# Kernel optimization log

Hardware: AMD Instinct MI355X
Metric: run time of the kernel (lower is better)

Reference implementation:

```python
import jax, jax.numpy as jnp
import numpy as np
from jax import lax

DEPTH = 3  # signature truncation depth
B, L, I, H, O = 256, 512, 32, 16, 10
SIG_DIM = H + H**2 + H**3  # 4368 = signatory.signature_channels(16, 3)


def setup_inputs() -> dict:
    key = jax.random.key(0)
    ks = jax.random.split(key, 7)
    s = 1.0 / np.sqrt(H).astype(np.float32)
    sf = 1.0 / np.sqrt(SIG_DIM).astype(np.float32)
    return {
        "X": jax.random.normal(ks[0], (B, L, I), jnp.float32),
        "W_ih": jax.random.uniform(ks[1], (4 * H, I), jnp.float32, -s, s),
        "W_hh": jax.random.uniform(ks[2], (4 * H, H), jnp.float32, -s, s),
        "b_ih": jax.random.uniform(ks[3], (4 * H,), jnp.float32, -s, s),
        "b_hh": jax.random.uniform(ks[4], (4 * H,), jnp.float32, -s, s),
        "fc_w": jax.random.uniform(ks[5], (O, SIG_DIM), jnp.float32, -sf, sf),
        "fc_b": jax.random.uniform(ks[6], (O,), jnp.float32, -sf, sf),
    }


def _lstm(X, W_ih, W_hh, b_ih, b_hh):
    # torch nn.LSTM, single layer, batch_first, gate order (i, f, g, o)
    b, l, _ = X.shape
    h0 = jnp.zeros((b, H), X.dtype)
    c0 = jnp.zeros((b, H), X.dtype)
    # precompute input projection for all timesteps: [L, B, 4H]
    xw = jnp.swapaxes(jnp.einsum('bli,gi->blg', X, W_ih) + b_ih + b_hh, 0, 1)

    def step(carry, xw_t):
        h, c = carry
        gates = xw_t + h @ W_hh.T
        i, f, g, o = jnp.split(gates, 4, axis=-1)
        c = jax.nn.sigmoid(f) * c + jax.nn.sigmoid(i) * jnp.tanh(g)
        h = jax.nn.sigmoid(o) * jnp.tanh(c)
        return (h, c), h

    _, hs = lax.scan(step, (h0, c0), xw)  # hs: [L, B, H]
    return jnp.swapaxes(hs, 0, 1)  # [B, L, H]


def _outer(a, b):
    # batched flattened tensor product: [B, m] x [B, n] -> [B, m*n]
    return (a[:, :, None] * b[:, None, :]).reshape(a.shape[0], -1)


def _signature(h, depth):
    # signatory.signature: Chen's identity scan over path increments,
    # returns concatenated levels 1..depth: [B, C + C^2 + ... + C^depth]
    b, l, c = h.shape
    dx = jnp.swapaxes(h[:, 1:] - h[:, :-1], 0, 1)  # [L-1, B, C]
    S0 = tuple(jnp.zeros((b, c ** (k + 1)), h.dtype) for k in range(depth))

    def step(S, d):
        # exp(d) levels: e_k = d^{tensor k} / k!
        e = [d]
        for k in range(2, depth + 1):
            e.append(_outer(e[-1], d) / k)
        # S <- S (x) exp(d), truncated:  newS_k = S_k + sum_{j=1..k-1} S_{k-j} (x) e_j + e_k
        newS = []
        for k in range(1, depth + 1):
            acc = S[k - 1] + e[k - 1]
            for j in range(1, k):
                acc = acc + _outer(S[k - j - 1], e[j - 1])
            newS.append(acc)
        return tuple(newS), None

    S, _ = lax.scan(step, S0, dx)
    return jnp.concatenate(S, axis=-1)  # [B, SIG_DIM]


def reference(X, W_ih, W_hh, b_ih, b_hh, fc_w, fc_b):
    hseq = _lstm(X, W_ih, W_hh, b_ih, b_hh)           # [B, L, H]
    sig = _signature(hseq, DEPTH)                      # [B, SIG_DIM]
    out = sig @ fc_w.T + fc_b                          # [B, O]
    return out.reshape(-1, O)
```

## Files before the change

### kernel.cpp

```cpp
#include <hip/hip_runtime.h>

#define NB 256
#define NL 512
#define NI 32
#define NH 16
#define NG 64
#define SIGD 4368
#define XS 516

__device__ __forceinline__ float RL(float v, int lane) {
  return __builtin_bit_cast(float, __builtin_amdgcn_readlane(__builtin_bit_cast(int, v), lane));
}
template<int CTRL>
__device__ __forceinline__ float QB(float v) {
  return __builtin_bit_cast(float, __builtin_amdgcn_update_dpp(
      0, __builtin_bit_cast(int, v), CTRL, 0xF, 0xF, true));
}
__device__ __forceinline__ int cutf(int k) {
  switch (k) {
    case 1: return 24;  case 2: return 102; case 3: return 180; case 4: return 258;
    case 5: return 335; case 6: return 412; case 7: return 488; case 8: return 511;
    default: return 0;
  }
}

__global__ __launch_bounds__(512, 1) void k_main(const float* __restrict__ X,
    const float* __restrict__ Wih, const float* __restrict__ bih,
    const float* __restrict__ bhh, const float* __restrict__ Whh,
    const float* __restrict__ fcw, const float* __restrict__ fcb,
    float* __restrict__ out) {
  __shared__ __align__(16) float xwT[NG * XS];
  __shared__ __align__(16) float bnd[144];
  __shared__ int prog;
  int tid = threadIdx.x;
  int wv = tid >> 6;
  int ln = tid & 63;
  int b = blockIdx.x;

  if (tid == 0) prog = -1;

  {
    const float Kg = (ln >= 32 && ln < 48) ? 2.885390082f : -1.442695041f;
    float w2[NI];
#pragma unroll
    for (int i = 0; i < 8; ++i) {
      float4 v = *(const float4*)(Wih + ln * NI + 4 * i);
      w2[4*i+0] = v.x; w2[4*i+1] = v.y; w2[4*i+2] = v.z; w2[4*i+3] = v.w;
    }
    float bias = bih[ln] + bhh[ln];
    const float* xb = X + (size_t)b * NL * NI;
#pragma unroll 4
    for (int t = 64 * wv; t < 64 * (wv + 1); ++t) {
      const float4* xr = (const float4*)(xb + t * NI);
      float x0 = bias, x1 = 0.f, x2 = 0.f, x3 = 0.f;
#pragma unroll
      for (int i = 0; i < 8; ++i) {
        float4 xv = xr[i];
        x0 += xv.x * w2[4*i+0]; x1 += xv.y * w2[4*i+1];
        x2 += xv.z * w2[4*i+2]; x3 += xv.w * w2[4*i+3];
      }
      xwT[ln * XS + t] = Kg * ((x0 + x1) + (x2 + x3));
    }
  }
  __syncthreads();

  if (wv == 0) {
    __asm__ __volatile__("s_setprio 3");
    const int q = ln & 3;
    const int j = ln >> 2;
    const int gmem = q * 16 + j;
    const bool isg = (q == 2);
    const float Kg = isg ? 2.885390082f : -1.442695041f;
    const float Av = isg ? -2.0f : 1.0f;
    const float Bv = isg ? 1.0f : 0.0f;
    const float CT = 2.885390082f;
    float w[NH];
#pragma unroll
    for (int qq = 0; qq < 4; ++qq) {
      float4 v = *(const float4*)(Whh + gmem * NH + 4 * qq);
      w[4*qq+0] = Kg*v.x; w[4*qq+1] = Kg*v.y; w[4*qq+2] = Kg*v.z; w[4*qq+3] = Kg*v.w;
    }
    const float* xt = xwT + gmem * XS;
    float4 xq[4];
#pragma unroll
    for (int i = 0; i < 4; ++i) xq[i] = *(const float4*)(xt + 4 * i);
    float cs = 0.0f, hval = 0.0f;
    for (int tb = 0; tb < NL; tb += 16) {
#pragma unroll
      for (int k = 0; k < 16; ++k) {
        int t = tb + k;
        float hs[16];
#pragma unroll
        for (int u = 0; u < 16; ++u) hs[u] = RL(hval, 4 * u);
        float xval = ((const float*)xq)[k];
        if ((k & 3) == 3 && t + 16 < NL)
          xq[k >> 2] = *(const float4*)(xt + (t + 13));
        float a0 = xval, a1 = 0.f, a2 = 0.f, a3 = 0.f;
#pragma unroll
        for (int u = 0; u < 4; ++u) {
          a0 += hs[4*u+0] * w[4*u+0];
          a1 += hs[4*u+1] * w[4*u+1];
          a2 += hs[4*u+2] * w[4*u+2];
          a3 += hs[4*u+3] * w[4*u+3];
        }
        float acc = (a0 + a1) + (a2 + a3);
        float e = __builtin_amdgcn_exp2f(acc);
        float r = __builtin_amdgcn_rcpf(1.0f + e);
        float val = __builtin_fmaf(Av, r, Bv);
        float iv = QB<0x00>(val);
        float fv = QB<0x55>(val);
        float gv = QB<0xAA>(val);
        float ov = QB<0xFF>(val);
        cs = __builtin_fmaf(fv, cs, (CT * iv) * gv);
        float e2 = __builtin_amdgcn_exp2f(cs);
        float tc = __builtin_fmaf(-2.0f, __builtin_amdgcn_rcpf(1.0f + e2), 1.0f);
        hval = ov * tc;
        if (q == 0) xwT[j * XS + t] = hval;
      }
      __asm__ __volatile__("" ::: "memory");
      if (ln == 0) *(volatile int*)&prog = tb + 15;
    }
    __asm__ __volatile__("s_setprio 0");
  }

  const int bi = ln & 15;
  const int hi = ln >> 4;
  const int ch = wv;
  int ts = cutf(ch);
  int te = cutf(ch + 1);
  while (*(volatile int*)&prog < te) __builtin_amdgcn_s_sleep(8);
  __asm__ __volatile__("" ::: "memory");

  float s3[4][16];
  float s2[4] = {0.f, 0.f, 0.f, 0.f};
#pragma unroll
  for (int m = 0; m < 4; ++m)
#pragma unroll
    for (int cc = 0; cc < 16; ++cc) s3[m][cc] = 0.f;
  float hc[16];
#pragma unroll
  for (int cc = 0; cc < 16; ++cc) hc[cc] = xwT[cc * XS + ts];
  float hcb = xwT[bi * XS + ts];
  float hca[4], h0a[4];
#pragma unroll
  for (int m = 0; m < 4; ++m) { hca[m] = xwT[(4 * m + hi) * XS + ts]; h0a[m] = hca[m]; }
  for (int t = ts; t < te; ++t) {
    int tn = t + 1;
    float hn[16];
#pragma unroll
    for (int cc = 0; cc < 16; ++cc) hn[cc] = xwT[cc * XS + tn];
    float hnb = xwT[bi * XS + tn];
    float d[16];
#pragma unroll
    for (int cc = 0; cc < 16; ++cc) d[cc] = hn[cc] - hc[cc];
    float db = hnb - hcb;
    float P[4];
#pragma unroll
    for (int m = 0; m < 4; ++m) {
      float hna = xwT[(4 * m + hi) * XS + tn];
      float da = hna - hca[m];
      float s1 = hca[m] - h0a[m];
      P[m] = s2[m] + db * (0.5f * s1 + 0.166666666667f * da);
      s2[m] += db * (s1 + 0.5f * da);
      hca[m] = hna;
    }
#pragma unroll
    for (int m = 0; m < 4; ++m)
#pragma unroll
      for (int cc = 0; cc < 16; ++cc)
        s3[m][cc] += P[m] * d[cc];
#pragma unroll
    for (int cc = 0; cc < 16; ++cc) hc[cc] = hn[cc];
    hcb = hnb;
  }
  __syncthreads();

  if (tid < 144) {
    int k = tid >> 4, j = tid & 15;
    bnd[tid] = xwT[j * XS + cutf(k)];
  }
  __syncthreads();

  float* slot0 = xwT;
  float* slot1 = xwT + 4352;
  float* sigb  = xwT + 8704;
  auto writeSlot = [&](float* slot) {
#pragma unroll
    for (int m = 0; m < 4; ++m) slot[64 * m + ln] = s2[m];
    float* s3s = slot + 256;
#pragma unroll
    for (int m = 0; m < 4; ++m)
#pragma unroll
      for (int cc = 0; cc < 16; ++cc)
        s3s[64 * ln + ((m * 16 + cc) ^ (ln & 31))] = s3[m][cc];
  };
  auto combineSlot = [&](const float* slot, int as_, int ae_, int bs_, int be_) {
    const float* s2b = slot;
    const float* s3b = slot + 256;
    float s1b[16];
#pragma unroll
    for (int cc = 0; cc < 16; ++cc) s1b[cc] = bnd[be_ * 16 + cc] - bnd[bs_ * 16 + cc];
    float s1bb = bnd[be_ * 16 + bi] - bnd[bs_ * 16 + bi];
    float s1aa[4];
#pragma unroll
    for (int m = 0; m < 4; ++m) {
      int a = 4 * m + hi;
      s1aa[m] = bnd[ae_ * 16 + a] - bnd[as_ * 16 + a];
    }
    float row[16];
#pragma unroll
    for (int cc = 0; cc < 16; ++cc) row[cc] = s2b[bi * 16 + cc];
#pragma unroll
    for (int m = 0; m < 4; ++m) {
      float s2bo = s2b[64 * m + ln];
#pragma unroll
      for (int cc = 0; cc < 16; ++cc)
        s3[m][cc] += s3b[64 * ln + ((m * 16 + cc) ^ (ln & 31))]
                   + s2[m] * s1b[cc] + s1aa[m] * row[cc];
      s2[m] += s2bo + s1aa[m] * s1bb;
    }
  };
  if (ch == 1) writeSlot(slot0);
  if (ch == 3) writeSlot(slot1);
  __syncthreads();
  if (ch == 0) combineSlot(slot0, 0, 1, 1, 2);
  if (ch == 2) combineSlot(slot1, 2, 3, 3, 4);
  __syncthreads();
  if (ch == 5) writeSlot(slot0);
  if (ch == 7) writeSlot(slot1);
  __syncthreads();
  if (ch == 4) combineSlot(slot0, 4, 5, 5, 6);
  if (ch == 6) combineSlot(slot1, 6, 7, 7, 8);
  __syncthreads();
  if (ch == 2) writeSlot(slot0);
  if (ch == 6) writeSlot(slot1);
  __syncthreads();
  if (ch == 0) combineSlot(slot0, 0, 2, 2, 4);
  if (ch == 4) combineSlot(slot1, 4, 6, 6, 8);
  __syncthreads();
  if (ch == 4) writeSlot(slot0);
  __syncthreads();
  if (ch == 0) {
    combineSlot(slot0, 0, 4, 4, 8);
    if (ln < 16) sigb[ln] = bnd[8 * 16 + ln] - bnd[ln];
#pragma unroll
    for (int m = 0; m < 4; ++m) sigb[16 + 64 * m + ln] = s2[m];
#pragma unroll
    for (int m = 0; m < 4; ++m) {
#pragma unroll
      for (int qq = 0; qq < 4; ++qq) {
        float4 v;
        v.x = s3[m][4*qq+0]; v.y = s3[m][4*qq+1]; v.z = s3[m][4*qq+2]; v.w = s3[m][4*qq+3];
        *(float4*)(sigb + 272 + 1024 * m + 256 * hi + 16 * bi + 4 * qq) = v;
      }
    }
  }
  __syncthreads();

  {
    float acc[10];
#pragma unroll
    for (int o = 0; o < 10; ++o) acc[o] = 0.f;
    for (int k = tid; k < SIGD; k += 512) {
      float s = sigb[k];
#pragma unroll
      for (int o = 0; o < 10; ++o) acc[o] += s * fcw[o * SIGD + k];
    }
#pragma unroll
    for (int o = 0; o < 10; ++o) {
      float v = acc[o];
#pragma unroll
      for (int off = 32; off > 0; off >>= 1) v += __shfl_down(v, off);
      if (ln == 0) bnd[wv * 10 + o] = v;
    }
    __syncthreads();
    if (tid < 10) {
      float s = fcb[tid];
#pragma unroll
      for (int w = 0; w < 8; ++w) s += bnd[w * 10 + tid];
      out[b * 10 + tid] = s;
    }
  }
}

extern "C" void kernel_launch(void* const* d_in, const int* in_sizes, int n_in,
                              void* d_out, int out_size, void* d_ws, size_t ws_size,
                              hipStream_t stream) {
  const float* X   = (const float*)d_in[0];
  const float* Wih = (const float*)d_in[1];
  const float* Whh = (const float*)d_in[2];
  const float* bih = (const float*)d_in[3];
  const float* bhh = (const float*)d_in[4];
  const float* fcw = (const float*)d_in[5];
  const float* fcb = (const float*)d_in[6];
  float* out = (float*)d_out;
  k_main<<<NB, 512, 0, stream>>>(X, Wih, bih, bhh, Whh, fcw, fcb, out);
}
```

Before: 195.6 us.

## Batch LSTM h stores, widen dot accumulators, remap signature chunks to waves

In the recurrent wave, the cell-state scale constant is folded into the sigmoid affine coefficient for the i gate. The dot product now uses eight independent accumulators to shorten dependency chains. Per-step scalar LDS stores of h are replaced by register buffering, with one float4 store per 16-step block spread across quads. The signature phase remaps chunk assignment so wave 0 (busy with the LSTM) takes the last chunk, and it double-buffers the h registers across an unrolled-by-two loop to avoid copies. This aims to shorten the serial LSTM critical path and let other waves start their signature chunks earlier, at the cost of more register pressure and somewhat more complex indexing.

```diff
diff --git a/kernel.cpp b/kernel.cpp
--- a/kernel.cpp
+++ b/kernel.cpp
@@ -71,9 +71,9 @@
     const int gmem = q * 16 + j;
     const bool isg = (q == 2);
     const float Kg = isg ? 2.885390082f : -1.442695041f;
-    const float Av = isg ? -2.0f : 1.0f;
+    const float CT = 2.885390082f;
+    const float Av = isg ? -2.0f : (q == 0 ? CT : 1.0f);
     const float Bv = isg ? 1.0f : 0.0f;
-    const float CT = 2.885390082f;
     float w[NH];
 #pragma unroll
     for (int qq = 0; qq < 4; ++qq) {
@@ -81,10 +81,12 @@
       w[4*qq+0] = Kg*v.x; w[4*qq+1] = Kg*v.y; w[4*qq+2] = Kg*v.z; w[4*qq+3] = Kg*v.w;
     }
     const float* xt = xwT + gmem * XS;
+    float* hdst = xwT + j * XS + 4 * q;
     float4 xq[4];
 #pragma unroll
     for (int i = 0; i < 4; ++i) xq[i] = *(const float4*)(xt + 4 * i);
     float cs = 0.0f, hval = 0.0f;
+    float hst[4] = {0.f, 0.f, 0.f, 0.f};
     for (int tb = 0; tb < NL; tb += 16) {
 #pragma unroll
       for (int k = 0; k < 16; ++k) {
@@ -96,14 +98,19 @@
         if ((k & 3) == 3 && t + 16 < NL)
           xq[k >> 2] = *(const float4*)(xt + (t + 13));
         float a0 = xval, a1 = 0.f, a2 = 0.f, a3 = 0.f;
-#pragma unroll
-        for (int u = 0; u < 4; ++u) {
-          a0 += hs[4*u+0] * w[4*u+0];
-          a1 += hs[4*u+1] * w[4*u+1];
-          a2 += hs[4*u+2] * w[4*u+2];
-          a3 += hs[4*u+3] * w[4*u+3];
+        float a4 = 0.f,  a5 = 0.f, a6 = 0.f, a7 = 0.f;
+#pragma unroll
+        for (int u = 0; u < 2; ++u) {
+          a0 += hs[8*u+0] * w[8*u+0];
+          a1 += hs[8*u+1] * w[8*u+1];
+          a2 += hs[8*u+2] * w[8*u+2];
+          a3 += hs[8*u+3] * w[8*u+3];
+          a4 += hs[8*u+4] * w[8*u+4];
+          a5 += hs[8*u+5] * w[8*u+5];
+          a6 += hs[8*u+6] * w[8*u+6];
+          a7 += hs[8*u+7] * w[8*u+7];
         }
-        float acc = (a0 + a1) + (a2 + a3);
+        float acc = ((a0 + a1) + (a2 + a3)) + ((a4 + a5) + (a6 + a7));
         float e = __builtin_amdgcn_exp2f(acc);
         float r = __builtin_amdgcn_rcpf(1.0f + e);
         float val = __builtin_fmaf(Av, r, Bv);
@@ -111,21 +118,27 @@
         float fv = QB<0x55>(val);
         float gv = QB<0xAA>(val);
         float ov = QB<0xFF>(val);
-        cs = __builtin_fmaf(fv, cs, (CT * iv) * gv);
+        cs = __builtin_fmaf(fv, cs, iv * gv);
         float e2 = __builtin_amdgcn_exp2f(cs);
         float tc = __builtin_fmaf(-2.0f, __builtin_amdgcn_rcpf(1.0f + e2), 1.0f);
         hval = ov * tc;
-        if (q == 0) xwT[j * XS + t] = hval;
+        hst[k & 3] = (q == (k >> 2)) ? hval : hst[k & 3];
       }
+      float4 hv;
+      hv.x = hst[0]; hv.y = hst[1]; hv.z = hst[2]; hv.w = hst[3];
+      *(float4*)(hdst + tb) = hv;
       __asm__ __volatile__("" ::: "memory");
       if (ln == 0) *(volatile int*)&prog = tb + 15;
     }
     __asm__ __volatile__("s_setprio 0");
   }
 
+  int ch = wv;
+  if (wv == 0) ch = 7;
+  else if (wv == 4) ch = 0;
+  else if (wv == 7) ch = 4;
   const int bi = ln & 15;
   const int hi = ln >> 4;
-  const int ch = wv;
   int ts = cutf(ch);
   int te = cutf(ch + 1);
   while (*(volatile int*)&prog < te) __builtin_amdgcn_s_sleep(8);
@@ -137,41 +150,48 @@
   for (int m = 0; m < 4; ++m)
 #pragma unroll
     for (int cc = 0; cc < 16; ++cc) s3[m][cc] = 0.f;
-  float hc[16];
-#pragma unroll
-  for (int cc = 0; cc < 16; ++cc) hc[cc] = xwT[cc * XS + ts];
-  float hcb = xwT[bi * XS + ts];
-  float hca[4], h0a[4];
-#pragma unroll
-  for (int m = 0; m < 4; ++m) { hca[m] = xwT[(4 * m + hi) * XS + ts]; h0a[m] = hca[m]; }
-  for (int t = ts; t < te; ++t) {
-    int tn = t + 1;
-    float hn[16];
-#pragma unroll
-    for (int cc = 0; cc < 16; ++cc) hn[cc] = xwT[cc * XS + tn];
-    float hnb = xwT[bi * XS + tn];
+
+  float hA[16], hB[16];
+  float hAb, hBb;
+  float hAa[4], hBa[4], h0a[4];
+#pragma unroll
+  for (int cc = 0; cc < 16; ++cc) hA[cc] = xwT[cc * XS + ts];
+  hAb = xwT[bi * XS + ts];
+#pragma unroll
+  for (int m = 0; m < 4; ++m) { hAa[m] = xwT[(4 * m + hi) * XS + ts]; h0a[m] = hAa[m]; }
+
+  auto SSTEP = [&](float (&hc16)[16], float& hcb, float (&hca)[4],
+                   float (&hn16)[16], float& hnb, float (&hna)[4], int tn) {
+#pragma unroll
+    for (int cc = 0; cc < 16; ++cc) hn16[cc] = xwT[cc * XS + tn];
+    hnb = xwT[bi * XS + tn];
     float d[16];
 #pragma unroll
-    for (int cc = 0; cc < 16; ++cc) d[cc] = hn[cc] - hc[cc];
+    for (int cc = 0; cc < 16; ++cc) d[cc] = hn16[cc] - hc16[cc];
     float db = hnb - hcb;
     float P[4];
 #pragma unroll
     for (int m = 0; m < 4; ++m) {
-      float hna = xwT[(4 * m + hi) * XS + tn];
-      float da = hna - hca[m];
+      hna[m] = xwT[(4 * m + hi) * XS + tn];
+      float da = hna[m] - hca[m];
       float s1 = hca[m] - h0a[m];
       P[m] = s2[m] + db * (0.5f * s1 + 0.166666666667f * da);
       s2[m] += db * (s1 + 0.5f * da);
-      hca[m] = hna;
     }
 #pragma unroll
     for (int m = 0; m < 4; ++m)
 #pragma unroll
       for (int cc = 0; cc < 16; ++cc)
         s3[m][cc] += P[m] * d[cc];
-#pragma unroll
-    for (int cc = 0; cc < 16; ++cc) hc[cc] = hn[cc];
-    hcb = hnb;
+  };
+
+  {
+    int t = ts;
+    for (; t + 2 <= te; t += 2) {
+      SSTEP(hA, hAb, hAa, hB, hBb, hBa, t + 1);
+      SSTEP(hB, hBb, hBa, hA, hAb, hAa, t + 2);
+    }
+    if (t < te) SSTEP(hA, hAb, hAa, hB, hBb, hBa, t + 1);
   }
   __syncthreads();
 
```

After: 196.4 us. About the same (+0.4%).
